# Performance work log

Hardware: AMD Instinct MI355X
Metric: run time of the kernel (lower is better)

Reference implementation:

```python
import jax, jax.numpy as jnp
import numpy as np

WS = 7          # window size
NH = 6          # heads per block
H = 112
W = 112
SHIFTS = (0, 3, 0, 3)  # alternating W-MSA / SW-MSA over depths=[2,2]


def _ln(x, g, b, eps=1e-5):
    m = x.mean(-1, keepdims=True)
    v = x.var(-1, keepdims=True)
    return (x - m) / jnp.sqrt(v + eps) * g + b


def _rel_idx():
    coords = np.stack(np.meshgrid(np.arange(WS), np.arange(WS), indexing='ij'))
    flat = coords.reshape(2, -1)
    rel = (flat[:, :, None] - flat[:, None, :]).transpose(1, 2, 0)
    rel[:, :, 0] += WS - 1
    rel[:, :, 1] += WS - 1
    rel[:, :, 0] *= 2 * WS - 1
    return rel.sum(-1)  # (49, 49) indices into the (2*WS-1)^2 bias table


def _attn_mask(shift):
    # standard Swin shifted-window attention mask, (nW, 49, 49)
    img = np.zeros((H, W))
    cnt = 0
    for hs in (slice(0, -WS), slice(-WS, -shift), slice(-shift, None)):
        for ws_ in (slice(0, -WS), slice(-WS, -shift), slice(-shift, None)):
            img[hs, ws_] = cnt
            cnt += 1
    win = img.reshape(H // WS, WS, W // WS, WS).transpose(0, 2, 1, 3).reshape(-1, WS * WS)
    m = win[:, None, :] - win[:, :, None]
    return np.where(m != 0, -100.0, 0.0).astype(np.float32)


def _win_part(x):  # (B,H,W,C) -> (B*nW, 49, C)
    B, _, _, C = x.shape
    x = x.reshape(B, H // WS, WS, W // WS, WS, C).transpose(0, 1, 3, 2, 4, 5)
    return x.reshape(-1, WS * WS, C)


def _win_rev(w, B, C):  # (B*nW, 49, C) -> (B,H,W,C)
    x = w.reshape(B, H // WS, W // WS, WS, WS, C).transpose(0, 1, 3, 2, 4, 5)
    return x.reshape(B, H, W, C)


def setup_inputs() -> dict:
    key = jax.random.key(0)
    ks = jax.random.split(key, 8)
    C, NB, B = 180, 4, 2
    f = lambda k, s: jax.random.normal(k, s, dtype=jnp.float32) * 0.02
    return {
        'x': jax.random.normal(ks[0], (B, C, H, W), dtype=jnp.float32),
        'pe_g': jnp.ones((C,), jnp.float32), 'pe_b': jnp.zeros((C,), jnp.float32),
        'ln1_g': jnp.ones((NB, C), jnp.float32), 'ln1_b': jnp.zeros((NB, C), jnp.float32),
        'qkv_w': f(ks[1], (NB, C, 3 * C)), 'qkv_b': jnp.zeros((NB, 3 * C), jnp.float32),
        'proj_w': f(ks[2], (NB, C, C)), 'proj_b': jnp.zeros((NB, C), jnp.float32),
        'ln2_g': jnp.ones((NB, C), jnp.float32), 'ln2_b': jnp.zeros((NB, C), jnp.float32),
        'fc1_w': f(ks[3], (NB, C, 4 * C)), 'fc1_b': jnp.zeros((NB, 4 * C), jnp.float32),
        'fc2_w': f(ks[4], (NB, 4 * C, C)), 'fc2_b': jnp.zeros((NB, C), jnp.float32),
        'rpb': f(ks[5], (NB, (2 * WS - 1) ** 2, NH)),
        'fn_g': jnp.ones((C,), jnp.float32), 'fn_b': jnp.zeros((C,), jnp.float32),
    }


def reference(x, pe_g, pe_b, ln1_g, ln1_b, qkv_w, qkv_b, proj_w, proj_b,
              ln2_g, ln2_b, fc1_w, fc1_b, fc2_w, fc2_b, rpb, fn_g, fn_b):
    B, C = x.shape[0], x.shape[1]
    dh = C // NH
    scale = dh ** -0.5
    rel_idx = jnp.asarray(_rel_idx())
    mask3 = jnp.asarray(_attn_mask(3))
    nW = (H // WS) * (W // WS)

    t = x.reshape(B, C, H * W).transpose(0, 2, 1)  # (B, L, C) tokens
    t = _ln(t, pe_g, pe_b)                          # patch_norm
    for i, shift in enumerate(SHIFTS):
        h = _ln(t, ln1_g[i], ln1_b[i]).reshape(B, H, W, C)
        if shift:
            h = jnp.roll(h, (-shift, -shift), axis=(1, 2))
        w = _win_part(h)                                            # (B*nW, 49, C)
        qkv = (w @ qkv_w[i] + qkv_b[i]).reshape(-1, WS * WS, 3, NH, dh)
        qkv = qkv.transpose(2, 0, 3, 1, 4)                          # (3, B*nW, NH, 49, dh)
        q, k, v = qkv[0] * scale, qkv[1], qkv[2]
        attn = jnp.einsum('bhid,bhjd->bhij', q, k)
        bias = rpb[i][rel_idx].transpose(2, 0, 1)                   # (NH, 49, 49)
        attn = attn + bias[None]
        if shift:
            attn = attn.reshape(B, nW, NH, WS * WS, WS * WS) + mask3[None, :, None]
            attn = attn.reshape(-1, NH, WS * WS, WS * WS)
        attn = jax.nn.softmax(attn, axis=-1)
        o = jnp.einsum('bhij,bhjd->bhid', attn, v)
        o = o.transpose(0, 2, 1, 3).reshape(-1, WS * WS, C)
        o = o @ proj_w[i] + proj_b[i]
        h = _win_rev(o, B, C)
        if shift:
            h = jnp.roll(h, (shift, shift), axis=(1, 2))
        t = t + h.reshape(B, H * W, C)                              # residual (drop_path=id at eval)
        m = _ln(t, ln2_g[i], ln2_b[i])
        m = jax.nn.gelu(m @ fc1_w[i] + fc1_b[i], approximate=False)
        t = t + (m @ fc2_w[i] + fc2_b[i])
    t = _ln(t, fn_g, fn_b)
    return t.reshape(B, H, W, C).transpose(0, 3, 1, 2)  # SwinBlock permute back to BCHW
```

## Files before the change

kernel.cpp:

```cpp
#include <hip/hip_runtime.h>
#include <hip/hip_bf16.h>
#include <cmath>

typedef __hip_bfloat16 bf16;
typedef short short8 __attribute__((ext_vector_type(8)));
typedef float f32x4  __attribute__((ext_vector_type(4)));

#define Cc    180
#define KP1   192
#define KP2   736
#define Hh    112
#define Wwid  112
#define Ltok  12544
#define Bsz   2
#define TOK   25088
#define WSz   7
#define NHd   6
#define DHd   30
#define NWIN  256
#define P49   49

__device__ __forceinline__ float LD(const void* p, size_t i, int f) {
    if (f) return ((const float*)p)[i];
    return (float)((const bf16*)p)[i];
}
__device__ __forceinline__ void ST(void* p, size_t i, int f, float v) {
    if (f) ((float*)p)[i] = v;
    else   ((bf16*)p)[i] = (bf16)v;
}

__device__ __forceinline__ float wred(float v) {
    v += __shfl_xor(v, 1);
    v += __shfl_xor(v, 2);
    v += __shfl_xor(v, 4);
    v += __shfl_xor(v, 8);
    v += __shfl_xor(v, 16);
    v += __shfl_xor(v, 32);
    return v;
}

__global__ void k_detect(const unsigned short* __restrict__ xb, int* __restrict__ flag) {
    __shared__ int s;
    if (threadIdx.x == 0) s = 0;
    __syncthreads();
    int bad = 0;
    for (int i = threadIdx.x; i < 2048; i += 256) {
        int e = (xb[i] >> 7) & 0xFF;
        if (e >= 0xC8) bad = 1;
    }
    if (bad) atomicOr(&s, 1);
    __syncthreads();
    if (threadIdx.x == 0) flag[0] = s;
}

__global__ __launch_bounds__(256) void k_tr(const void* __restrict__ src, size_t woff,
                                            bf16* __restrict__ dst,
                                            int K, int N, int Kp, int Npad,
                                            const int* __restrict__ dflag) {
    int f = *dflag;
    int idx = blockIdx.x * 256 + threadIdx.x;
    if (idx >= Npad * Kp) return;
    int n = idx / Kp, k = idx % Kp;
    float v = (n < N && k < K) ? LD(src, woff + (size_t)k * N + n, f) : 0.f;
    dst[idx] = (bf16)v;
}

__global__ __launch_bounds__(256) void k_trq(const void* __restrict__ src, size_t woff,
                                             bf16* __restrict__ dst,
                                             const int* __restrict__ dflag) {
    int f = *dflag;
    int idx = blockIdx.x * 256 + threadIdx.x;
    if (idx >= 576 * KP1) return;
    int n = idx / KP1, k = idx % KP1;
    int sec = n / 192, rm = n % 192, hd = rm >> 5, d = rm & 31;
    float v = (d < 30 && k < 180) ? LD(src, woff + (size_t)k * 540 + sec * 180 + hd * 30 + d, f) : 0.f;
    dst[idx] = (bf16)v;
}

__global__ __launch_bounds__(256) void k_bias(const void* __restrict__ rpb, size_t off,
                                              float* __restrict__ BT,
                                              const int* __restrict__ dflag) {
    int f = *dflag;
    int idx = blockIdx.x * 256 + threadIdx.x;
    if (idx >= NHd * 4096) return;
    int hd = idx >> 12, rem = idx & 4095;
    int i = rem >> 6, j = rem & 63;
    float v;
    if (i < 49 && j < 49) {
        int rel = (i / 7 - j / 7 + 6) * 13 + (i % 7 - j % 7 + 6);
        v = LD(rpb, off + (size_t)rel * NHd + hd, f);
    } else {
        v = -1.0e9f;
    }
    BT[idx] = v;
}

__global__ __launch_bounds__(256) void k_patchnorm(const void* __restrict__ x,
                                                   const void* __restrict__ g,
                                                   const void* __restrict__ b,
                                                   float* __restrict__ T,
                                                   const int* __restrict__ dflag) {
    int f = *dflag;
    int tokid = blockIdx.x * 4 + (threadIdx.x >> 6);
    int lane  = threadIdx.x & 63;
    int bb = tokid / Ltok, ll = tokid % Ltok;
    size_t base = (size_t)bb * Cc * Ltok + ll;
    float v0 = LD(x, base + (size_t)lane * Ltok, f);
    float v1 = LD(x, base + (size_t)(lane + 64) * Ltok, f);
    float v2 = (lane < 52) ? LD(x, base + (size_t)(lane + 128) * Ltok, f) : 0.f;
    float s  = wred(v0 + v1 + v2);
    float sq = wred(v0 * v0 + v1 * v1 + v2 * v2);
    float mean = s * (1.f / 180.f);
    float var  = sq * (1.f / 180.f) - mean * mean;
    float rstd = rsqrtf(var + 1e-5f);
    float* tp = T + (size_t)tokid * Cc;
    tp[lane]      = (v0 - mean) * rstd * LD(g, lane, f)      + LD(b, lane, f);
    tp[lane + 64] = (v1 - mean) * rstd * LD(g, lane + 64, f) + LD(b, lane + 64, f);
    if (lane < 52)
        tp[lane + 128] = (v2 - mean) * rstd * LD(g, lane + 128, f) + LD(b, lane + 128, f);
}

__global__ __launch_bounds__(256) void k_ln(const float* __restrict__ T,
                                            const void* __restrict__ g,
                                            const void* __restrict__ b,
                                            bf16* __restrict__ D,
                                            int windowed, int shift, int goff,
                                            const int* __restrict__ dflag) {
    int f = *dflag;
    int r    = blockIdx.x * 4 + (threadIdx.x >> 6);
    int lane = threadIdx.x & 63;
    int src;
    if (windowed) {
        int bb  = r / (NWIN * P49);
        int rem = r % (NWIN * P49);
        int wi = rem / P49, p = rem % P49;
        int wy = wi >> 4, wx = wi & 15;
        int py = p / 7, px = p % 7;
        int gh = (wy * 7 + py + shift) % Hh;
        int gw = (wx * 7 + px + shift) % Wwid;
        src = bb * Ltok + gh * Wwid + gw;
    } else {
        src = r;
    }
    const float* tp = T + (size_t)src * Cc;
    float v0 = tp[lane];
    float v1 = tp[lane + 64];
    float v2 = (lane < 52) ? tp[lane + 128] : 0.f;
    float s  = wred(v0 + v1 + v2);
    float sq = wred(v0 * v0 + v1 * v1 + v2 * v2);
    float mean = s * (1.f / 180.f);
    float var  = sq * (1.f / 180.f) - mean * mean;
    float rstd = rsqrtf(var + 1e-5f);
    bf16* dp = D + (size_t)r * KP1;
    dp[lane]      = (bf16)((v0 - mean) * rstd * LD(g, goff + lane, f)      + LD(b, goff + lane, f));
    dp[lane + 64] = (bf16)((v1 - mean) * rstd * LD(g, goff + lane + 64, f) + LD(b, goff + lane + 64, f));
    if (lane < 52)
        dp[lane + 128] = (bf16)((v2 - mean) * rstd * LD(g, goff + lane + 128, f) + LD(b, goff + lane + 128, f));
    else
        dp[lane + 128] = (bf16)0.f;
}

__global__ __launch_bounds__(256) void k_final(const float* __restrict__ T,
                                               const void* __restrict__ g,
                                               const void* __restrict__ b,
                                               void* __restrict__ out,
                                               const int* __restrict__ dflag) {
    int f = *dflag;
    int tokid = blockIdx.x * 4 + (threadIdx.x >> 6);
    int lane  = threadIdx.x & 63;
    int bb = tokid / Ltok, ll = tokid % Ltok;
    const float* tp = T + (size_t)tokid * Cc;
    float v0 = tp[lane];
    float v1 = tp[lane + 64];
    float v2 = (lane < 52) ? tp[lane + 128] : 0.f;
    float s  = wred(v0 + v1 + v2);
    float sq = wred(v0 * v0 + v1 * v1 + v2 * v2);
    float mean = s * (1.f / 180.f);
    float var  = sq * (1.f / 180.f) - mean * mean;
    float rstd = rsqrtf(var + 1e-5f);
    size_t base = (size_t)bb * Cc * Ltok + ll;
    ST(out, base + (size_t)lane * Ltok,        f, (v0 - mean) * rstd * LD(g, lane, f)      + LD(b, lane, f));
    ST(out, base + (size_t)(lane + 64) * Ltok, f, (v1 - mean) * rstd * LD(g, lane + 64, f) + LD(b, lane + 64, f));
    if (lane < 52)
        ST(out, base + (size_t)(lane + 128) * Ltok, f,
           (v2 - mean) * rstd * LD(g, lane + 128, f) + LD(b, lane + 128, f));
}

template <int EPI>
__global__ __launch_bounds__(256) void k_mgemm(const bf16* __restrict__ A,
                                               const bf16* __restrict__ Wt,
                                               const void* __restrict__ bias,
                                               size_t boff, int Nbias,
                                               bf16* __restrict__ OutB, int ldOut, int Nstore,
                                               float* __restrict__ OutF,
                                               bf16* __restrict__ Vt,
                                               int Kp, int shift, int rowoff,
                                               const int* __restrict__ dflag) {
    __shared__ __align__(16) short Als[8 * 64 * 8];
    __shared__ __align__(16) short Bls[4 * 64 * 8];
    int tid  = threadIdx.x;
    int lane = tid & 63;
    int w    = tid >> 6;
    int wr   = w >> 1, wc = w & 1;
    int m0 = blockIdx.y * 128;
    int n0 = blockIdx.x * 64;
    int m_lo = lane & 15, q = lane >> 4;

    f32x4 acc[4][2] = {};

    for (int k0 = 0; k0 < Kp; k0 += 32) {
#pragma unroll
        for (int s = 0; s < 2; ++s) {
            int ri = tid + s * 256;
            int mt = ri >> 6, ln = ri & 63;
            const bf16* src = A + (size_t)(m0 + mt * 16 + (ln & 15)) * Kp + k0 + (ln >> 4) * 8;
            *(ulonglong2*)(&Als[ri * 8]) = *(const ulonglong2*)src;
        }
        {
            int ri = tid;
            int nt = ri >> 6, ln = ri & 63;
            const bf16* src = Wt + (size_t)(n0 + nt * 16 + (ln & 15)) * Kp + k0 + (ln >> 4) * 8;
            *(ulonglong2*)(&Bls[ri * 8]) = *(const ulonglong2*)src;
        }
        __syncthreads();
        short8 b0 = *(const short8*)&Bls[((wc * 2 + 0) * 64 + lane) * 8];
        short8 b1 = *(const short8*)&Bls[((wc * 2 + 1) * 64 + lane) * 8];
#pragma unroll
        for (int mt = 0; mt < 4; ++mt) {
            short8 a = *(const short8*)&Als[((wr * 4 + mt) * 64 + lane) * 8];
            acc[mt][0] = __builtin_amdgcn_mfma_f32_16x16x32_bf16(a, b0, acc[mt][0], 0, 0, 0);
            acc[mt][1] = __builtin_amdgcn_mfma_f32_16x16x32_bf16(a, b1, acc[mt][1], 0, 0, 0);
        }
        __syncthreads();
    }

    int f = *dflag;
#pragma unroll
    for (int mt = 0; mt < 4; ++mt) {
#pragma unroll
        for (int nt = 0; nt < 2; ++nt) {
#pragma unroll
            for (int r = 0; r < 4; ++r) {
                int row = m0 + (wr * 4 + mt) * 16 + q * 4 + r;
                int col = n0 + (wc * 2 + nt) * 16 + m_lo;
                float val = acc[mt][nt][r];
                if (EPI == 1) {
                    float bv = (col < Nbias) ? LD(bias, boff + col, f) : 0.f;
                    val += bv;
                    val = 0.5f * val * (1.f + erff(val * 0.70710678118654752f));
                    if (col < Nstore) OutB[(size_t)row * ldOut + col] = (bf16)val;
                } else if (EPI == 2) {
                    if (col < Nstore)
                        OutF[(size_t)(rowoff + row) * Cc + col] += val + LD(bias, boff + col, f);
                } else if (EPI == 3) {
                    if (col < Nstore) {
                        int grow = rowoff + row;
                        int bb  = grow / (NWIN * P49);
                        int rem = grow % (NWIN * P49);
                        int wi = rem / P49, p = rem % P49;
                        int wy = wi >> 4, wx = wi & 15;
                        int py = p / 7, px = p % 7;
                        int gh = (wy * 7 + py + shift) % Hh;
                        int gw = (wx * 7 + px + shift) % Wwid;
                        int tgt = bb * Ltok + gh * Wwid + gw;
                        OutF[(size_t)tgt * Cc + col] += val + LD(bias, boff + col, f);
                    }
                } else {
                    int sec = col / 192, rm = col % 192;
                    int hd = rm >> 5, d = rm & 31;
                    float bv = (d < 30) ? LD(bias, boff + sec * 180 + hd * 30 + d, f) : 0.f;
                    val += bv;
                    if (sec == 0) val *= 0.18257418583505536f;
                    if (sec < 2) {
                        OutB[(size_t)row * 384 + sec * 192 + hd * 32 + d] = (bf16)val;
                    } else {
                        int wloc = row / 49, p = row % 49;
                        Vt[(((size_t)wloc * NHd + hd) * 32 + d) * 64 + p] = (bf16)val;
                    }
                }
            }
        }
    }
}

__device__ __forceinline__ int regionOf(int g, int shift) {
    return (g < Hh - WSz) ? 0 : ((g < Hh - shift) ? 1 : 2);
}

__global__ __launch_bounds__(64) void k_mattn(const bf16* __restrict__ QK,
                                              const bf16* __restrict__ Vt,
                                              const float* __restrict__ BT,
                                              bf16* __restrict__ Ow,
                                              int shift, int w0) {
    __shared__ __align__(16) bf16 P[64 * 72];
    int lane = threadIdx.x;
    int lw = blockIdx.x / NHd, hd = blockIdx.x % NHd;
    int r0 = lw * P49;
    int q = lane >> 4, c = lane & 15;

    const bf16* qb = QK + (size_t)(r0 + c) * 384 + hd * 32 + q * 8;
    short8 qf[4], kf[4];
#pragma unroll
    for (int t = 0; t < 4; ++t) {
        qf[t] = *(const short8*)(qb + (size_t)t * 16 * 384);
        kf[t] = *(const short8*)(qb + 192 + (size_t)t * 16 * 384);
    }
    f32x4 zero = {0.f, 0.f, 0.f, 0.f};
    f32x4 S[4][4];
#pragma unroll
    for (int mt = 0; mt < 4; ++mt)
#pragma unroll
        for (int nt = 0; nt < 4; ++nt)
            S[mt][nt] = __builtin_amdgcn_mfma_f32_16x16x32_bf16(qf[mt], kf[nt], zero, 0, 0, 0);

    const float* bt = BT + hd * 4096;
    int wi = (w0 + lw) & (NWIN - 1);
    int wy = wi >> 4, wx = wi & 15;
    int lj[4], li[4][4];
    if (shift) {
#pragma unroll
        for (int nt = 0; nt < 4; ++nt) {
            int j = nt * 16 + c;
            lj[nt] = (j < 49) ? regionOf(wy * 7 + j / 7, shift) * 3 + regionOf(wx * 7 + j % 7, shift) : -1;
        }
#pragma unroll
        for (int mt = 0; mt < 4; ++mt)
#pragma unroll
            for (int r = 0; r < 4; ++r) {
                int i = mt * 16 + q * 4 + r;
                li[mt][r] = (i < 49) ? regionOf(wy * 7 + i / 7, shift) * 3 + regionOf(wx * 7 + i % 7, shift) : -2;
            }
    }
    float rmax[4][4];
#pragma unroll
    for (int mt = 0; mt < 4; ++mt)
#pragma unroll
        for (int r = 0; r < 4; ++r) rmax[mt][r] = -3.0e38f;
#pragma unroll
    for (int mt = 0; mt < 4; ++mt)
#pragma unroll
        for (int nt = 0; nt < 4; ++nt)
#pragma unroll
            for (int r = 0; r < 4; ++r) {
                int i = mt * 16 + q * 4 + r, j = nt * 16 + c;
                float v = S[mt][nt][r] + bt[i * 64 + j];
                if (shift && li[mt][r] != lj[nt]) v -= 100.f;
                S[mt][nt][r] = v;
                rmax[mt][r] = fmaxf(rmax[mt][r], v);
            }
#pragma unroll
    for (int mt = 0; mt < 4; ++mt)
#pragma unroll
        for (int r = 0; r < 4; ++r) {
            float m = rmax[mt][r];
            m = fmaxf(m, __shfl_xor(m, 1));
            m = fmaxf(m, __shfl_xor(m, 2));
            m = fmaxf(m, __shfl_xor(m, 4));
            m = fmaxf(m, __shfl_xor(m, 8));
            rmax[mt][r] = m;
        }
    float rsum[4][4] = {};
#pragma unroll
    for (int mt = 0; mt < 4; ++mt)
#pragma unroll
        for (int nt = 0; nt < 4; ++nt)
#pragma unroll
            for (int r = 0; r < 4; ++r) {
                float e = __expf(S[mt][nt][r] - rmax[mt][r]);
                S[mt][nt][r] = e;
                rsum[mt][r] += e;
            }
#pragma unroll
    for (int mt = 0; mt < 4; ++mt)
#pragma unroll
        for (int r = 0; r < 4; ++r) {
            float s = rsum[mt][r];
            s += __shfl_xor(s, 1);
            s += __shfl_xor(s, 2);
            s += __shfl_xor(s, 4);
            s += __shfl_xor(s, 8);
            rsum[mt][r] = 1.f / s;
        }
#pragma unroll
    for (int mt = 0; mt < 4; ++mt)
#pragma unroll
        for (int nt = 0; nt < 4; ++nt)
#pragma unroll
            for (int r = 0; r < 4; ++r)
                P[(mt * 16 + q * 4 + r) * 72 + nt * 16 + c] = (bf16)(S[mt][nt][r] * rsum[mt][r]);
    __syncthreads();

    f32x4 O[4][2] = {};
    const bf16* vb = Vt + (((size_t)lw * NHd + hd) * 32 + c) * 64 + q * 8;
#pragma unroll
    for (int ks = 0; ks < 2; ++ks) {
        short8 vf0 = *(const short8*)(vb + ks * 32);
        short8 vf1 = *(const short8*)(vb + 16 * 64 + ks * 32);
#pragma unroll
        for (int mt = 0; mt < 4; ++mt) {
            short8 pf = *(const short8*)&P[(mt * 16 + c) * 72 + ks * 32 + q * 8];
            O[mt][0] = __builtin_amdgcn_mfma_f32_16x16x32_bf16(pf, vf0, O[mt][0], 0, 0, 0);
            O[mt][1] = __builtin_amdgcn_mfma_f32_16x16x32_bf16(pf, vf1, O[mt][1], 0, 0, 0);
        }
    }
    int r0g = (w0 + lw) * P49;
#pragma unroll
    for (int mt = 0; mt < 4; ++mt)
#pragma unroll
        for (int nt = 0; nt < 2; ++nt)
#pragma unroll
            for (int r = 0; r < 4; ++r) {
                int i = mt * 16 + q * 4 + r, d = nt * 16 + c;
                if (i < 49 && d < 30)
                    Ow[(size_t)(r0g + i) * KP1 + hd * 30 + d] = (bf16)O[mt][nt][r];
            }
    if (hd == 0) {
        for (int idx = lane; idx < P49 * 12; idx += 64) {
            int p = idx / 12, cp = 180 + idx % 12;
            Ow[(size_t)(r0g + p) * KP1 + cp] = (bf16)0.f;
        }
    }
}

extern "C" void kernel_launch(void* const* d_in, const int* in_sizes, int n_in,
                              void* d_out, int out_size, void* d_ws, size_t ws_size,
                              hipStream_t stream) {
    const void* x      = d_in[0];
    const void* pe_g   = d_in[1];
    const void* pe_b   = d_in[2];
    const void* ln1_g  = d_in[3];
    const void* ln1_b  = d_in[4];
    const void* qkv_w  = d_in[5];
    const void* qkv_b  = d_in[6];
    const void* proj_w = d_in[7];
    const void* proj_b = d_in[8];
    const void* ln2_g  = d_in[9];
    const void* ln2_b  = d_in[10];
    const void* fc1_w  = d_in[11];
    const void* fc1_b  = d_in[12];
    const void* fc2_w  = d_in[13];
    const void* fc2_b  = d_in[14];
    const void* rpb    = d_in[15];
    const void* fn_g   = d_in[16];
    const void* fn_b   = d_in[17];

    const size_t wtQ = (size_t)576 * KP1, wtP = (size_t)192 * KP1;
    const size_t wtF1 = (size_t)768 * KP1, wtF2 = (size_t)192 * KP2;
    const size_t wtPerBlk = wtQ + wtP + wtF1 + wtF2;

    int*   dflag = (int*)d_ws;
    float* T     = (float*)((char*)d_ws + 256);
    bf16*  Abuf  = (bf16*)(T + (size_t)TOK * Cc);
    bf16*  Wts   = Abuf + (size_t)TOK * KP1;
    float* BT    = (float*)(Wts + 4 * wtPerBlk);
    bf16*  Vt    = (bf16*)(BT + NHd * 4096);
    size_t fixed = (size_t)((char*)Vt - (char*)d_ws);

    int c = 1;
    while (c < 4 && fixed + ((size_t)(Bsz * NWIN / c) * NHd * 32 * 64
                             + (size_t)(TOK / c) * KP2) * 2 > ws_size) c <<= 1;
    int CM = TOK / c;
    int CW = (Bsz * NWIN) / c;
    bf16* Bbuf = Vt + (size_t)CW * NHd * 32 * 64;

    dim3 b256(256);
    k_detect<<<1, b256, 0, stream>>>((const unsigned short*)x, dflag);

    for (int i = 0; i < 4; ++i) {
        bf16* wq  = Wts + i * wtPerBlk;
        bf16* wp  = wq + wtQ;
        bf16* wf1 = wp + wtP;
        bf16* wf2 = wf1 + wtF1;
        k_trq<<<(int)((wtQ + 255) / 256), b256, 0, stream>>>(qkv_w, (size_t)i * Cc * 540, wq, dflag);
        k_tr<<<(int)((wtP  + 255) / 256), b256, 0, stream>>>(proj_w, (size_t)i * Cc * Cc,  wp,  180, 180, KP1, 192, dflag);
        k_tr<<<(int)((wtF1 + 255) / 256), b256, 0, stream>>>(fc1_w,  (size_t)i * Cc * 720, wf1, 180, 720, KP1, 768, dflag);
        k_tr<<<(int)((wtF2 + 255) / 256), b256, 0, stream>>>(fc2_w,  (size_t)i * 720 * Cc, wf2, 720, 180, KP2, 192, dflag);
    }

    k_patchnorm<<<TOK / 4, b256, 0, stream>>>(x, pe_g, pe_b, T, dflag);

    const int shifts[4] = {0, 3, 0, 3};
    for (int i = 0; i < 4; ++i) {
        int sh = shifts[i];
        bf16* wq  = Wts + i * wtPerBlk;
        bf16* wp  = wq + wtQ;
        bf16* wf1 = wp + wtP;
        bf16* wf2 = wf1 + wtF1;

        k_bias<<<(NHd * 4096 + 255) / 256, b256, 0, stream>>>(rpb, (size_t)i * 169 * NHd, BT, dflag);
        k_ln<<<TOK / 4, b256, 0, stream>>>(T, ln1_g, ln1_b, Abuf, 1, sh, i * Cc, dflag);
        for (int j = 0; j < c; ++j) {
            int R0 = j * CM;
            dim3 g1(576 / 64, CM / 128);
            k_mgemm<4><<<g1, b256, 0, stream>>>(Abuf + (size_t)R0 * KP1, wq, qkv_b,
                                                (size_t)i * 540, 540, Bbuf, 384, 576,
                                                nullptr, Vt, KP1, 0, 0, dflag);
            k_mattn<<<CW * NHd, 64, 0, stream>>>(Bbuf, Vt, BT, Abuf, sh, j * CW);
            dim3 g2(192 / 64, CM / 128);
            k_mgemm<3><<<g2, b256, 0, stream>>>(Abuf + (size_t)R0 * KP1, wp, proj_b,
                                                (size_t)i * Cc, Cc, nullptr, 0, Cc,
                                                T, nullptr, KP1, sh, R0, dflag);
        }
        k_ln<<<TOK / 4, b256, 0, stream>>>(T, ln2_g, ln2_b, Abuf, 0, 0, i * Cc, dflag);
        for (int j = 0; j < c; ++j) {
            int R0 = j * CM;
            dim3 g3(768 / 64, CM / 128);
            k_mgemm<1><<<g3, b256, 0, stream>>>(Abuf + (size_t)R0 * KP1, wf1, fc1_b,
                                                (size_t)i * 720, 720, Bbuf, KP2, KP2,
                                                nullptr, nullptr, KP1, 0, 0, dflag);
            dim3 g4(192 / 64, CM / 128);
            k_mgemm<2><<<g4, b256, 0, stream>>>(Bbuf, wf2, fc2_b,
                                                (size_t)i * Cc, Cc, nullptr, 0, Cc,
                                                T, nullptr, KP2, 0, R0, dflag);
        }
    }

    k_final<<<TOK / 4, b256, 0, stream>>>(T, fn_g, fn_b, d_out, dflag);
}
```

Measured before the change: 950.4 us.

## Restructure MFMA GEMM to stage weights in LDS and stream A from global

Replaces the per-32-K-step GEMM, which staged both A and B tiles through LDS with two barriers each step, by a kernel that loads up to 256 K-columns of the weight tile into LDS at once. Each wave reads its A fragments straight from global memory and computes a 16*MT x 64 strip. K is now a template constant so the loop can be unrolled. This cuts barrier count and LDS traffic for A, but A loads become uncoalesced per-wave global reads with no reuse across waves, and the larger MT=4 variants raise register pressure.

```diff
diff --git a/kernel.cpp b/kernel.cpp
--- a/kernel.cpp
+++ b/kernel.cpp
@@ -186,63 +186,56 @@
            (v2 - mean) * rstd * LD(g, lane + 128, f) + LD(b, lane + 128, f));
 }
 
-template <int EPI>
-__global__ __launch_bounds__(256) void k_mgemm(const bf16* __restrict__ A,
+template <int EPI, int MT, int KPT>
+__global__ __launch_bounds__(256) void k_sgemm(const bf16* __restrict__ A,
                                                const bf16* __restrict__ Wt,
                                                const void* __restrict__ bias,
                                                size_t boff, int Nbias,
                                                bf16* __restrict__ OutB, int ldOut, int Nstore,
                                                float* __restrict__ OutF,
                                                bf16* __restrict__ Vt,
-                                               int Kp, int shift, int rowoff,
+                                               int shift, int rowoff,
                                                const int* __restrict__ dflag) {
-    __shared__ __align__(16) short Als[8 * 64 * 8];
-    __shared__ __align__(16) short Bls[4 * 64 * 8];
-    int tid  = threadIdx.x;
-    int lane = tid & 63;
-    int w    = tid >> 6;
-    int wr   = w >> 1, wc = w & 1;
-    int m0 = blockIdx.y * 128;
+    __shared__ __align__(16) short Bls[8 * 4 * 64 * 8];
+    int tid = threadIdx.x, lane = tid & 63, w = tid >> 6;
+    int q = lane >> 4, c = lane & 15;
     int n0 = blockIdx.x * 64;
-    int m_lo = lane & 15, q = lane >> 4;
-
-    f32x4 acc[4][2] = {};
-
-    for (int k0 = 0; k0 < Kp; k0 += 32) {
-#pragma unroll
-        for (int s = 0; s < 2; ++s) {
-            int ri = tid + s * 256;
-            int mt = ri >> 6, ln = ri & 63;
-            const bf16* src = A + (size_t)(m0 + mt * 16 + (ln & 15)) * Kp + k0 + (ln >> 4) * 8;
-            *(ulonglong2*)(&Als[ri * 8]) = *(const ulonglong2*)src;
-        }
-        {
-            int ri = tid;
-            int nt = ri >> 6, ln = ri & 63;
-            const bf16* src = Wt + (size_t)(n0 + nt * 16 + (ln & 15)) * Kp + k0 + (ln >> 4) * 8;
-            *(ulonglong2*)(&Bls[ri * 8]) = *(const ulonglong2*)src;
-        }
+    int mw = blockIdx.y * (64 * MT) + w * (16 * MT);
+    f32x4 acc[MT][4] = {};
+
+    for (int k0 = 0; k0 < KPT; k0 += 256) {
+        const int nst = (KPT - k0 >= 256) ? 8 : ((KPT - k0) >> 5);
+        if (k0) __syncthreads();
+#pragma unroll
+        for (int s = 0; s < nst; ++s)
+            *(ulonglong2*)&Bls[(((s << 2) + w) * 64 + lane) * 8] =
+                *(const ulonglong2*)(Wt + (size_t)(n0 + w * 16 + c) * KPT + k0 + s * 32 + q * 8);
         __syncthreads();
-        short8 b0 = *(const short8*)&Bls[((wc * 2 + 0) * 64 + lane) * 8];
-        short8 b1 = *(const short8*)&Bls[((wc * 2 + 1) * 64 + lane) * 8];
-#pragma unroll
-        for (int mt = 0; mt < 4; ++mt) {
-            short8 a = *(const short8*)&Als[((wr * 4 + mt) * 64 + lane) * 8];
-            acc[mt][0] = __builtin_amdgcn_mfma_f32_16x16x32_bf16(a, b0, acc[mt][0], 0, 0, 0);
-            acc[mt][1] = __builtin_amdgcn_mfma_f32_16x16x32_bf16(a, b1, acc[mt][1], 0, 0, 0);
-        }
-        __syncthreads();
-    }
-
-    int f = *dflag;
-#pragma unroll
-    for (int mt = 0; mt < 4; ++mt) {
-#pragma unroll
-        for (int nt = 0; nt < 2; ++nt) {
+#pragma unroll
+        for (int s = 0; s < nst; ++s) {
+            short8 bfr[4];
+#pragma unroll
+            for (int nt = 0; nt < 4; ++nt)
+                bfr[nt] = *(const short8*)&Bls[(((s << 2) + nt) * 64 + lane) * 8];
+#pragma unroll
+            for (int mt = 0; mt < MT; ++mt) {
+                short8 af = *(const short8*)(A + (size_t)(mw + mt * 16 + c) * KPT + k0 + s * 32 + q * 8);
+#pragma unroll
+                for (int nt = 0; nt < 4; ++nt)
+                    acc[mt][nt] = __builtin_amdgcn_mfma_f32_16x16x32_bf16(af, bfr[nt], acc[mt][nt], 0, 0, 0);
+            }
+        }
+    }
+
+    int f = *dflag;
+#pragma unroll
+    for (int mt = 0; mt < MT; ++mt) {
+#pragma unroll
+        for (int nt = 0; nt < 4; ++nt) {
 #pragma unroll
             for (int r = 0; r < 4; ++r) {
-                int row = m0 + (wr * 4 + mt) * 16 + q * 4 + r;
-                int col = n0 + (wc * 2 + nt) * 16 + m_lo;
+                int row = mw + mt * 16 + q * 4 + r;
+                int col = n0 + nt * 16 + c;
                 float val = acc[mt][nt][r];
                 if (EPI == 1) {
                     float bv = (col < Nbias) ? LD(bias, boff + col, f) : 0.f;
@@ -480,6 +473,7 @@
     k_patchnorm<<<TOK / 4, b256, 0, stream>>>(x, pe_g, pe_b, T, dflag);
 
     const int shifts[4] = {0, 3, 0, 3};
+    bool m256 = (CM % 256) == 0;
     for (int i = 0; i < 4; ++i) {
         int sh = shifts[i];
         bf16* wq  = Wts + i * wtPerBlk;
@@ -491,27 +485,33 @@
         k_ln<<<TOK / 4, b256, 0, stream>>>(T, ln1_g, ln1_b, Abuf, 1, sh, i * Cc, dflag);
         for (int j = 0; j < c; ++j) {
             int R0 = j * CM;
-            dim3 g1(576 / 64, CM / 128);
-            k_mgemm<4><<<g1, b256, 0, stream>>>(Abuf + (size_t)R0 * KP1, wq, qkv_b,
-                                                (size_t)i * 540, 540, Bbuf, 384, 576,
-                                                nullptr, Vt, KP1, 0, 0, dflag);
+            if (m256)
+                k_sgemm<4, 4, KP1><<<dim3(9, CM / 256), b256, 0, stream>>>(
+                    Abuf + (size_t)R0 * KP1, wq, qkv_b, (size_t)i * 540, 540,
+                    Bbuf, 384, 576, nullptr, Vt, 0, 0, dflag);
+            else
+                k_sgemm<4, 2, KP1><<<dim3(9, CM / 128), b256, 0, stream>>>(
+                    Abuf + (size_t)R0 * KP1, wq, qkv_b, (size_t)i * 540, 540,
+                    Bbuf, 384, 576, nullptr, Vt, 0, 0, dflag);
             k_mattn<<<CW * NHd, 64, 0, stream>>>(Bbuf, Vt, BT, Abuf, sh, j * CW);
-            dim3 g2(192 / 64, CM / 128);
-            k_mgemm<3><<<g2, b256, 0, stream>>>(Abuf + (size_t)R0 * KP1, wp, proj_b,
-                                                (size_t)i * Cc, Cc, nullptr, 0, Cc,
-                                                T, nullptr, KP1, sh, R0, dflag);
+            k_sgemm<3, 2, KP1><<<dim3(3, CM / 128), b256, 0, stream>>>(
+                Abuf + (size_t)R0 * KP1, wp, proj_b, (size_t)i * Cc, Cc,
+                nullptr, 0, Cc, T, nullptr, sh, R0, dflag);
         }
         k_ln<<<TOK / 4, b256, 0, stream>>>(T, ln2_g, ln2_b, Abuf, 0, 0, i * Cc, dflag);
         for (int j = 0; j < c; ++j) {
             int R0 = j * CM;
-            dim3 g3(768 / 64, CM / 128);
-            k_mgemm<1><<<g3, b256, 0, stream>>>(Abuf + (size_t)R0 * KP1, wf1, fc1_b,
-                                                (size_t)i * 720, 720, Bbuf, KP2, KP2,
-                                                nullptr, nullptr, KP1, 0, 0, dflag);
-            dim3 g4(192 / 64, CM / 128);
-            k_mgemm<2><<<g4, b256, 0, stream>>>(Bbuf, wf2, fc2_b,
-                                                (size_t)i * Cc, Cc, nullptr, 0, Cc,
-                                                T, nullptr, KP2, 0, R0, dflag);
+            if (m256)
+                k_sgemm<1, 4, KP1><<<dim3(12, CM / 256), b256, 0, stream>>>(
+                    Abuf + (size_t)R0 * KP1, wf1, fc1_b, (size_t)i * 720, 720,
+                    Bbuf, KP2, KP2, nullptr, nullptr, 0, 0, dflag);
+            else
+                k_sgemm<1, 2, KP1><<<dim3(12, CM / 128), b256, 0, stream>>>(
+                    Abuf + (size_t)R0 * KP1, wf1, fc1_b, (size_t)i * 720, 720,
+                    Bbuf, KP2, KP2, nullptr, nullptr, 0, 0, dflag);
+            k_sgemm<2, 2, KP2><<<dim3(3, CM / 128), b256, 0, stream>>>(
+                Bbuf, wf2, fc2_b, (size_t)i * Cc, Cc,
+                nullptr, 0, Cc, T, nullptr, 0, R0, dflag);
         }
     }
 
```

Result: slower. 1.053 ms (+10.8%).

## Stage GEMM epilogues through LDS, prefetch operands, drop V transpose buffer

Applied to the files above, without the earlier changes.

The GEMM kernel now prefetches the next K-slice of A and W into registers while the current slice runs through the MFMAs. Its epilogue stages results in shared memory, so stores go out as coalesced 16-byte bf16 writes or float4 read-modify-writes on the residual. QKV output is written as a plain 576-wide row, and the attention kernel transposes V into LDS itself instead of reading a separately scattered Vt buffer. The relative-position bias tables for all four blocks are built once up front. The cost is an extra LDS pass and two more barriers in the epilogue, plus extra LDS use in the attention kernel.

```diff
diff --git a/kernel.cpp b/kernel.cpp
--- a/kernel.cpp
+++ b/kernel.cpp
@@ -29,6 +29,14 @@
     else   ((bf16*)p)[i] = (bf16)v;
 }
 
+__device__ __forceinline__ short bh(float x) { bf16 t = (bf16)x; return *(short*)&t; }
+__device__ __forceinline__ short8 cvt8(float4 a, float4 b) {
+    short8 o;
+    o[0] = bh(a.x); o[1] = bh(a.y); o[2] = bh(a.z); o[3] = bh(a.w);
+    o[4] = bh(b.x); o[5] = bh(b.y); o[6] = bh(b.z); o[7] = bh(b.w);
+    return o;
+}
+
 __device__ __forceinline__ float wred(float v) {
     v += __shfl_xor(v, 1);
     v += __shfl_xor(v, 2);
@@ -77,18 +85,20 @@
     dst[idx] = (bf16)v;
 }
 
-__global__ __launch_bounds__(256) void k_bias(const void* __restrict__ rpb, size_t off,
+__global__ __launch_bounds__(256) void k_bias(const void* __restrict__ rpb,
                                               float* __restrict__ BT,
                                               const int* __restrict__ dflag) {
     int f = *dflag;
     int idx = blockIdx.x * 256 + threadIdx.x;
-    if (idx >= NHd * 4096) return;
-    int hd = idx >> 12, rem = idx & 4095;
+    if (idx >= 4 * NHd * 4096) return;
+    int blk = idx / (NHd * 4096);
+    int rem0 = idx % (NHd * 4096);
+    int hd = rem0 >> 12, rem = rem0 & 4095;
     int i = rem >> 6, j = rem & 63;
     float v;
     if (i < 49 && j < 49) {
         int rel = (i / 7 - j / 7 + 6) * 13 + (i % 7 - j % 7 + 6);
-        v = LD(rpb, off + (size_t)rel * NHd + hd, f);
+        v = LD(rpb, (size_t)blk * 169 * NHd + (size_t)rel * NHd + hd, f);
     } else {
         v = -1.0e9f;
     }
@@ -193,36 +203,38 @@
                                                size_t boff, int Nbias,
                                                bf16* __restrict__ OutB, int ldOut, int Nstore,
                                                float* __restrict__ OutF,
-                                               bf16* __restrict__ Vt,
                                                int Kp, int shift, int rowoff,
                                                const int* __restrict__ dflag) {
-    __shared__ __align__(16) short Als[8 * 64 * 8];
-    __shared__ __align__(16) short Bls[4 * 64 * 8];
-    int tid  = threadIdx.x;
-    int lane = tid & 63;
-    int w    = tid >> 6;
-    int wr   = w >> 1, wc = w & 1;
-    int m0 = blockIdx.y * 128;
-    int n0 = blockIdx.x * 64;
-    int m_lo = lane & 15, q = lane >> 4;
-
+    __shared__ __align__(16) char SM[64 * 72 * 4];
+    short* Als = (short*)SM;
+    short* Bls = (short*)(SM + 8192);
+    float* Els = (float*)SM;
+    int tid = threadIdx.x, lane = tid & 63, w = tid >> 6;
+    int wr = w >> 1, wc = w & 1;
+    int q = lane >> 4, c = lane & 15;
+    int m0 = blockIdx.y * 128, n0 = blockIdx.x * 64;
     f32x4 acc[4][2] = {};
 
+    int rowA0 = m0 + (tid >> 6) * 16 + (tid & 15);
+    int rowW  = n0 + (tid >> 6) * 16 + (tid & 15);
+    int koff  = ((tid >> 4) & 3) * 8;
+    const bf16* pa0 = A + (size_t)rowA0 * Kp + koff;
+    const bf16* pa1 = A + (size_t)(rowA0 + 64) * Kp + koff;
+    const bf16* pw  = Wt + (size_t)rowW * Kp + koff;
+    ulonglong2 rA0 = *(const ulonglong2*)pa0;
+    ulonglong2 rA1 = *(const ulonglong2*)pa1;
+    ulonglong2 rW  = *(const ulonglong2*)pw;
+
     for (int k0 = 0; k0 < Kp; k0 += 32) {
-#pragma unroll
-        for (int s = 0; s < 2; ++s) {
-            int ri = tid + s * 256;
-            int mt = ri >> 6, ln = ri & 63;
-            const bf16* src = A + (size_t)(m0 + mt * 16 + (ln & 15)) * Kp + k0 + (ln >> 4) * 8;
-            *(ulonglong2*)(&Als[ri * 8]) = *(const ulonglong2*)src;
-        }
-        {
-            int ri = tid;
-            int nt = ri >> 6, ln = ri & 63;
-            const bf16* src = Wt + (size_t)(n0 + nt * 16 + (ln & 15)) * Kp + k0 + (ln >> 4) * 8;
-            *(ulonglong2*)(&Bls[ri * 8]) = *(const ulonglong2*)src;
-        }
+        *(ulonglong2*)&Als[tid * 8]         = rA0;
+        *(ulonglong2*)&Als[(tid + 256) * 8] = rA1;
+        *(ulonglong2*)&Bls[tid * 8]         = rW;
         __syncthreads();
+        if (k0 + 32 < Kp) {
+            rA0 = *(const ulonglong2*)(pa0 + k0 + 32);
+            rA1 = *(const ulonglong2*)(pa1 + k0 + 32);
+            rW  = *(const ulonglong2*)(pw  + k0 + 32);
+        }
         short8 b0 = *(const short8*)&Bls[((wc * 2 + 0) * 64 + lane) * 8];
         short8 b1 = *(const short8*)&Bls[((wc * 2 + 1) * 64 + lane) * 8];
 #pragma unroll
@@ -236,25 +248,58 @@
 
     int f = *dflag;
 #pragma unroll
-    for (int mt = 0; mt < 4; ++mt) {
-#pragma unroll
-        for (int nt = 0; nt < 2; ++nt) {
-#pragma unroll
-            for (int r = 0; r < 4; ++r) {
-                int row = m0 + (wr * 4 + mt) * 16 + q * 4 + r;
-                int col = n0 + (wc * 2 + nt) * 16 + m_lo;
-                float val = acc[mt][nt][r];
-                if (EPI == 1) {
-                    float bv = (col < Nbias) ? LD(bias, boff + col, f) : 0.f;
-                    val += bv;
-                    val = 0.5f * val * (1.f + erff(val * 0.70710678118654752f));
-                    if (col < Nstore) OutB[(size_t)row * ldOut + col] = (bf16)val;
-                } else if (EPI == 2) {
-                    if (col < Nstore)
-                        OutF[(size_t)(rowoff + row) * Cc + col] += val + LD(bias, boff + col, f);
-                } else if (EPI == 3) {
-                    if (col < Nstore) {
-                        int grow = rowoff + row;
+    for (int Ph = 0; Ph < 2; ++Ph) {
+        if (Ph) __syncthreads();
+        if (wr == Ph) {
+#pragma unroll
+            for (int mt = 0; mt < 4; ++mt)
+#pragma unroll
+                for (int nt = 0; nt < 2; ++nt)
+#pragma unroll
+                    for (int r = 0; r < 4; ++r) {
+                        int rl = mt * 16 + q * 4 + r;
+                        int cl = (wc * 2 + nt) * 16 + c;
+                        int col = n0 + cl;
+                        float val = acc[mt][nt][r];
+                        if (EPI == 4) {
+                            int sec = col / 192, rm = col % 192;
+                            int hd = rm >> 5, d = rm & 31;
+                            if (d < 30) val += LD(bias, boff + sec * 180 + hd * 30 + d, f);
+                            if (sec == 0) val *= 0.18257418583505536f;
+                        } else if (EPI == 1) {
+                            if (col < Nbias) val += LD(bias, boff + col, f);
+                            val = 0.5f * val * (1.f + erff(val * 0.70710678118654752f));
+                        } else {
+                            if (col < Nstore) val += LD(bias, boff + col, f);
+                        }
+                        Els[rl * 72 + cl] = val;
+                    }
+        }
+        __syncthreads();
+        if (EPI == 1 || EPI == 4) {
+#pragma unroll
+            for (int it = 0; it < 2; ++it) {
+                int ri = it * 256 + tid;
+                int row = ri >> 3, c8 = ri & 7;
+                int gcol = n0 + c8 * 8;
+                if (gcol < Nstore) {
+                    float4 v0 = *(float4*)&Els[row * 72 + c8 * 8];
+                    float4 v1 = *(float4*)&Els[row * 72 + c8 * 8 + 4];
+                    short8 o = cvt8(v0, v1);
+                    *(ulonglong2*)(OutB + (size_t)(m0 + Ph * 64 + row) * ldOut + gcol) =
+                        *(ulonglong2*)&o;
+                }
+            }
+        } else {
+#pragma unroll
+            for (int it = 0; it < 4; ++it) {
+                int ri = it * 256 + tid;
+                int row = ri >> 4, c4 = ri & 15;
+                int col = n0 + c4 * 4;
+                if (col < Nstore) {
+                    int grow = rowoff + m0 + Ph * 64 + row;
+                    int tgt = grow;
+                    if (EPI == 3) {
                         int bb  = grow / (NWIN * P49);
                         int rem = grow % (NWIN * P49);
                         int wi = rem / P49, p = rem % P49;
@@ -262,21 +307,13 @@
                         int py = p / 7, px = p % 7;
                         int gh = (wy * 7 + py + shift) % Hh;
                         int gw = (wx * 7 + px + shift) % Wwid;
-                        int tgt = bb * Ltok + gh * Wwid + gw;
-                        OutF[(size_t)tgt * Cc + col] += val + LD(bias, boff + col, f);
+                        tgt = bb * Ltok + gh * Wwid + gw;
                     }
-                } else {
-                    int sec = col / 192, rm = col % 192;
-                    int hd = rm >> 5, d = rm & 31;
-                    float bv = (d < 30) ? LD(bias, boff + sec * 180 + hd * 30 + d, f) : 0.f;
-                    val += bv;
-                    if (sec == 0) val *= 0.18257418583505536f;
-                    if (sec < 2) {
-                        OutB[(size_t)row * 384 + sec * 192 + hd * 32 + d] = (bf16)val;
-                    } else {
-                        int wloc = row / 49, p = row % 49;
-                        Vt[(((size_t)wloc * NHd + hd) * 32 + d) * 64 + p] = (bf16)val;
-                    }
+                    float4* tp = (float4*)(OutF + (size_t)tgt * Cc + col);
+                    float4 t = *tp;
+                    float4 e = *(float4*)&Els[row * 72 + c4 * 4];
+                    t.x += e.x; t.y += e.y; t.z += e.z; t.w += e.w;
+                    *tp = t;
                 }
             }
         }
@@ -287,24 +324,37 @@
     return (g < Hh - WSz) ? 0 : ((g < Hh - shift) ? 1 : 2);
 }
 
-__global__ __launch_bounds__(64) void k_mattn(const bf16* __restrict__ QK,
-                                              const bf16* __restrict__ Vt,
+__global__ __launch_bounds__(64) void k_mattn(const bf16* __restrict__ QKV,
+                                              const bf16* __restrict__ Vt_unused,
                                               const float* __restrict__ BT,
                                               bf16* __restrict__ Ow,
                                               int shift, int w0) {
     __shared__ __align__(16) bf16 P[64 * 72];
+    __shared__ __align__(16) bf16 Vl[32 * 72];
     int lane = threadIdx.x;
     int lw = blockIdx.x / NHd, hd = blockIdx.x % NHd;
     int r0 = lw * P49;
     int q = lane >> 4, c = lane & 15;
 
-    const bf16* qb = QK + (size_t)(r0 + c) * 384 + hd * 32 + q * 8;
+    const bf16* qb = QKV + (size_t)(r0 + c) * 576 + hd * 32 + q * 8;
     short8 qf[4], kf[4];
 #pragma unroll
     for (int t = 0; t < 4; ++t) {
-        qf[t] = *(const short8*)(qb + (size_t)t * 16 * 384);
-        kf[t] = *(const short8*)(qb + 192 + (size_t)t * 16 * 384);
-    }
+        qf[t] = *(const short8*)(qb + (size_t)t * 16 * 576);
+        kf[t] = *(const short8*)(qb + 192 + (size_t)t * 16 * 576);
+    }
+    for (int t = lane; t < 32 * 15; t += 64) {
+        int d = t / 15, p = 49 + t % 15;
+        Vl[d * 72 + p] = (bf16)0.f;
+    }
+    for (int t = lane; t < P49 * 4; t += 64) {
+        int p = t >> 2, ch = t & 3;
+        ulonglong2 v = *(const ulonglong2*)(QKV + (size_t)(r0 + p) * 576 + 384 + hd * 32 + ch * 8);
+        bf16* vv = (bf16*)&v;
+#pragma unroll
+        for (int j = 0; j < 8; ++j) Vl[(ch * 8 + j) * 72 + p] = vv[j];
+    }
+
     f32x4 zero = {0.f, 0.f, 0.f, 0.f};
     f32x4 S[4][4];
 #pragma unroll
@@ -391,11 +441,10 @@
     __syncthreads();
 
     f32x4 O[4][2] = {};
-    const bf16* vb = Vt + (((size_t)lw * NHd + hd) * 32 + c) * 64 + q * 8;
 #pragma unroll
     for (int ks = 0; ks < 2; ++ks) {
-        short8 vf0 = *(const short8*)(vb + ks * 32);
-        short8 vf1 = *(const short8*)(vb + 16 * 64 + ks * 32);
+        short8 vf0 = *(const short8*)&Vl[(0  + c) * 72 + ks * 32 + q * 8];
+        short8 vf1 = *(const short8*)&Vl[(16 + c) * 72 + ks * 32 + q * 8];
 #pragma unroll
         for (int mt = 0; mt < 4; ++mt) {
             short8 pf = *(const short8*)&P[(mt * 16 + c) * 72 + ks * 32 + q * 8];
@@ -452,16 +501,14 @@
     float* T     = (float*)((char*)d_ws + 256);
     bf16*  Abuf  = (bf16*)(T + (size_t)TOK * Cc);
     bf16*  Wts   = Abuf + (size_t)TOK * KP1;
-    float* BT    = (float*)(Wts + 4 * wtPerBlk);
-    bf16*  Vt    = (bf16*)(BT + NHd * 4096);
-    size_t fixed = (size_t)((char*)Vt - (char*)d_ws);
+    float* BT4   = (float*)(Wts + 4 * wtPerBlk);
+    bf16*  Bbuf  = (bf16*)(BT4 + 4 * NHd * 4096);
+    size_t fixed = (size_t)((char*)Bbuf - (char*)d_ws);
 
     int c = 1;
-    while (c < 4 && fixed + ((size_t)(Bsz * NWIN / c) * NHd * 32 * 64
-                             + (size_t)(TOK / c) * KP2) * 2 > ws_size) c <<= 1;
+    while (c < 4 && fixed + (size_t)(TOK / c) * KP2 * 2 > ws_size) c <<= 1;
     int CM = TOK / c;
     int CW = (Bsz * NWIN) / c;
-    bf16* Bbuf = Vt + (size_t)CW * NHd * 32 * 64;
 
     dim3 b256(256);
     k_detect<<<1, b256, 0, stream>>>((const unsigned short*)x, dflag);
@@ -476,6 +523,7 @@
         k_tr<<<(int)((wtF1 + 255) / 256), b256, 0, stream>>>(fc1_w,  (size_t)i * Cc * 720, wf1, 180, 720, KP1, 768, dflag);
         k_tr<<<(int)((wtF2 + 255) / 256), b256, 0, stream>>>(fc2_w,  (size_t)i * 720 * Cc, wf2, 720, 180, KP2, 192, dflag);
     }
+    k_bias<<<(4 * NHd * 4096 + 255) / 256, b256, 0, stream>>>(rpb, BT4, dflag);
 
     k_patchnorm<<<TOK / 4, b256, 0, stream>>>(x, pe_g, pe_b, T, dflag);
 
@@ -487,31 +535,27 @@
         bf16* wf1 = wp + wtP;
         bf16* wf2 = wf1 + wtF1;
 
-        k_bias<<<(NHd * 4096 + 255) / 256, b256, 0, stream>>>(rpb, (size_t)i * 169 * NHd, BT, dflag);
         k_ln<<<TOK / 4, b256, 0, stream>>>(T, ln1_g, ln1_b, Abuf, 1, sh, i * Cc, dflag);
         for (int j = 0; j < c; ++j) {
             int R0 = j * CM;
-            dim3 g1(576 / 64, CM / 128);
-            k_mgemm<4><<<g1, b256, 0, stream>>>(Abuf + (size_t)R0 * KP1, wq, qkv_b,
-                                                (size_t)i * 540, 540, Bbuf, 384, 576,
-                                                nullptr, Vt, KP1, 0, 0, dflag);
-            k_mattn<<<CW * NHd, 64, 0, stream>>>(Bbuf, Vt, BT, Abuf, sh, j * CW);
-            dim3 g2(192 / 64, CM / 128);
-            k_mgemm<3><<<g2, b256, 0, stream>>>(Abuf + (size_t)R0 * KP1, wp, proj_b,
-                                                (size_t)i * Cc, Cc, nullptr, 0, Cc,
-                                                T, nullptr, KP1, sh, R0, dflag);
+            k_mgemm<4><<<dim3(9, CM / 128), b256, 0, stream>>>(
+                Abuf + (size_t)R0 * KP1, wq, qkv_b, (size_t)i * 540, 540,
+                Bbuf, 576, 576, nullptr, KP1, 0, 0, dflag);
+            k_mattn<<<CW * NHd, 64, 0, stream>>>(Bbuf, nullptr, BT4 + i * NHd * 4096,
+                                                 Abuf, sh, j * CW);
+            k_mgemm<3><<<dim3(3, CM / 128), b256, 0, stream>>>(
+                Abuf + (size_t)R0 * KP1, wp, proj_b, (size_t)i * Cc, Cc,
+                nullptr, 0, Cc, T, KP1, sh, R0, dflag);
         }
         k_ln<<<TOK / 4, b256, 0, stream>>>(T, ln2_g, ln2_b, Abuf, 0, 0, i * Cc, dflag);
         for (int j = 0; j < c; ++j) {
             int R0 = j * CM;
-            dim3 g3(768 / 64, CM / 128);
-            k_mgemm<1><<<g3, b256, 0, stream>>>(Abuf + (size_t)R0 * KP1, wf1, fc1_b,
-                                                (size_t)i * 720, 720, Bbuf, KP2, KP2,
-                                                nullptr, nullptr, KP1, 0, 0, dflag);
-            dim3 g4(192 / 64, CM / 128);
-            k_mgemm<2><<<g4, b256, 0, stream>>>(Bbuf, wf2, fc2_b,
-                                                (size_t)i * Cc, Cc, nullptr, 0, Cc,
-                                                T, nullptr, KP2, 0, R0, dflag);
+            k_mgemm<1><<<dim3(12, CM / 128), b256, 0, stream>>>(
+                Abuf + (size_t)R0 * KP1, wf1, fc1_b, (size_t)i * 720, 720,
+                Bbuf, KP2, KP2, nullptr, KP1, 0, 0, dflag);
+            k_mgemm<2><<<dim3(3, CM / 128), b256, 0, stream>>>(
+                Bbuf, wf2, fc2_b, (size_t)i * Cc, Cc,
+                nullptr, 0, Cc, T, KP2, 0, R0, dflag);
         }
     }
 
```

Measured after the change: 941.5 us. No clear change (-0.9%).
